# Performance work log

Hardware: AMD Instinct MI355X
Metric: run time of the kernel (lower is better)

## Reference

```python
import jax, jax.numpy as jnp
import numpy as np

B, T, C, H = 128, 256, 512, 512

def setup_inputs() -> dict:
    key = jax.random.key(0)
    k1, k2, k3, k4 = jax.random.split(key, 4)
    x = jax.random.normal(k1, (B, T, C), dtype=jnp.float32)
    # nn.Linear(n_embed, H_size, bias=False).weight has shape [H, C]; scaled init
    s = 1.0 / np.sqrt(C)
    Wq = jax.random.normal(k2, (H, C), dtype=jnp.float32) * s
    Wk = jax.random.normal(k3, (H, C), dtype=jnp.float32) * s
    Wv = jax.random.normal(k4, (H, C), dtype=jnp.float32) * s
    return {"x": x, "Wq": Wq, "Wk": Wk, "Wv": Wv}

def reference(x, Wq, Wk, Wv):
    # q,k,v: [B,T,H] = x @ W.T (torch Linear convention)
    q = jnp.einsum('btc,hc->bth', x, Wq)
    k = jnp.einsum('btc,hc->bth', x, Wk)
    v = jnp.einsum('btc,hc->bth', x, Wv)
    scale = k.shape[-1] ** -0.5
    score = jnp.einsum('bqh,bkh->bqk', q, k) * scale  # [B,T,T]
    # causal mask: position j attends to i only if i <= j
    i = jnp.arange(T)
    causal = i[None, :] <= i[:, None]  # [T,T] lower-triangular
    score = jnp.where(causal[None, :, :], score, -jnp.inf)
    attn = jax.nn.softmax(score, axis=-1)
    # dropout is identity in eval mode
    out = jnp.einsum('bqk,bkh->bqh', attn, v)  # [B,T,H]
    return out
```

## Files before the change

kernel.cpp:

```cpp
#include <hip/hip_runtime.h>

#define B_ 128
#define T_ 256
#define C_ 512
#define H_ 512
#define CSCALE 0.063763824f

typedef _Float16 f16x8 __attribute__((ext_vector_type(8)));
typedef _Float16 f16x4 __attribute__((ext_vector_type(4)));
typedef _Float16 f16x2 __attribute__((ext_vector_type(2)));
typedef float    f32x4 __attribute__((ext_vector_type(4)));
typedef float    f32x16 __attribute__((ext_vector_type(16)));
typedef unsigned int u32;
typedef u32 u32x4 __attribute__((ext_vector_type(4)));

__device__ __forceinline__ void gld16(const void* gsrc, void* ldst) {
  __builtin_amdgcn_global_load_lds(
      (__attribute__((address_space(1))) void*)gsrc,
      (__attribute__((address_space(3))) void*)ldst, 16, 0, 0);
}

__global__ __launch_bounds__(256) void cvtx_kernel(
    const float4* __restrict__ x, f16x4* __restrict__ dst) {
  const int NX = (B_ * T_ * C_) / 4;
  int gid = blockIdx.x * 256 + threadIdx.x;
  int gsz = gridDim.x * 256;
  for (int i = gid; i < NX; i += gsz) {
    float4 f = x[i];
    f16x4 u = {(_Float16)f.x, (_Float16)f.y, (_Float16)f.z, (_Float16)f.w};
    dst[i] = u;
  }
}

__global__ __launch_bounds__(256) void cvtw_kernel(
    const float4* __restrict__ wq, const float4* __restrict__ wk,
    const float4* __restrict__ wv, f16x4* __restrict__ dst) {
  const int NW = (H_ * C_) / 4;
  int i = blockIdx.x * 256 + threadIdx.x;
  if (i >= 3 * NW) return;
  float4 f = (i < NW) ? wq[i] : (i < 2 * NW ? wk[i - NW] : wv[i - 2 * NW]);
  f16x4 u = {(_Float16)f.x, (_Float16)f.y, (_Float16)f.z, (_Float16)f.w};
  dst[i] = u;
}

__global__ __launch_bounds__(256) void proj_kernel(
    const _Float16* __restrict__ xh, const _Float16* __restrict__ wh,
    _Float16* __restrict__ qh, _Float16* __restrict__ kh,
    _Float16* __restrict__ vth) {
  __shared__ _Float16 As[128 * 32];
  __shared__ _Float16 Bs[128 * 32];

  const int tid  = threadIdx.x;
  const int lane = tid & 63;
  const int wave = tid >> 6;
  const int lr = lane & 15, lk = lane >> 4;
  const int m0 = blockIdx.x * 128;
  const int n0 = blockIdx.y * 128;
  const int z  = blockIdx.z;
  const _Float16* wz = wh + z * (H_ * C_);

  const int wm = (wave >> 1) * 64;
  const int wn = (wave & 1) * 64;

  f32x4 acc[4][4];
#pragma unroll
  for (int i = 0; i < 4; ++i)
#pragma unroll
    for (int j = 0; j < 4; ++j) acc[i][j] = {0.f, 0.f, 0.f, 0.f};

  const int srow = tid >> 2, scol = (tid & 3) * 8;
  const _Float16* aSrc = xh + (size_t)(m0 + srow) * C_ + scol;
  const _Float16* bSrc = wz + (size_t)(n0 + srow) * C_ + scol;

  for (int k0 = 0; k0 < C_; k0 += 32) {
    __syncthreads();
#pragma unroll
    for (int i = 0; i < 2; ++i) {
      gld16((const void*)(aSrc + i * 64 * C_ + k0), (void*)&As[i * 2048 + wave * 512]);
      gld16((const void*)(bSrc + i * 64 * C_ + k0), (void*)&Bs[i * 2048 + wave * 512]);
    }
    __syncthreads();

    f16x8 a[4], b[4];
#pragma unroll
    for (int mi = 0; mi < 4; ++mi)
      a[mi] = *(const f16x8*)&As[(wm + mi * 16 + lr) * 32 + lk * 8];
#pragma unroll
    for (int ni = 0; ni < 4; ++ni)
      b[ni] = *(const f16x8*)&Bs[(wn + ni * 16 + lr) * 32 + lk * 8];
#pragma unroll
    for (int mi = 0; mi < 4; ++mi)
#pragma unroll
      for (int ni = 0; ni < 4; ++ni)
        acc[mi][ni] = __builtin_amdgcn_mfma_f32_16x16x32_f16(a[mi], b[ni], acc[mi][ni], 0, 0, 0);
  }

  if (z < 2) {
    _Float16* out = (z == 0) ? qh : kh;
#pragma unroll
    for (int mi = 0; mi < 4; ++mi) {
      int mbase = m0 + wm + mi * 16 + lk * 4;
#pragma unroll
      for (int ni = 0; ni < 4; ++ni) {
        int n = n0 + wn + ni * 16 + lr;
#pragma unroll
        for (int r = 0; r < 4; ++r)
          out[(size_t)(mbase + r) * H_ + n] = (_Float16)acc[mi][ni][r];
      }
    }
  } else {
#pragma unroll
    for (int mi = 0; mi < 4; ++mi) {
      int mbase = m0 + wm + mi * 16 + lk * 4;
      int bb = mbase >> 8, tt = mbase & 255;
#pragma unroll
      for (int ni = 0; ni < 4; ++ni) {
        int n = n0 + wn + ni * 16 + lr;
        f16x4 u = {(_Float16)acc[mi][ni][0], (_Float16)acc[mi][ni][1],
                   (_Float16)acc[mi][ni][2], (_Float16)acc[mi][ni][3]};
        *(f16x4*)&vth[(size_t)bb * (H_ * T_) + (size_t)n * T_ + tt] = u;
      }
    }
  }
}

__global__ __launch_bounds__(256, 3) void attn_kernel(
    const _Float16* __restrict__ qh, const _Float16* __restrict__ kh,
    const _Float16* __restrict__ vth, float* __restrict__ dout) {
  __shared__ f32x4 Ex[2][4][4][64];

  const int tid  = threadIdx.x;
  const int lane = tid & 63;
  const int wq   = tid >> 6;
  const int lq   = lane & 31;
  const int hi   = lane >> 5;
  const int flat = blockIdx.x;
  const int xcd  = flat & 7;
  const int rest = flat >> 3;
  const int qb   = 7 - (rest & 7);
  const int g    = rest >> 3;
  const int b    = xcd + (g << 3);
  const int q0   = qb * 32;
  const int nkv  = qb + 1;
  const int hbase = wq * 128;
  const int qg   = q0 + lq;

  f16x8 qf[8];
  const _Float16* qp = qh + ((size_t)b * T_ + qg) * H_ + hbase + hi * 8;
#pragma unroll
  for (int ks = 0; ks < 8; ++ks) qf[ks] = *(const f16x8*)&qp[ks * 16];

  f32x16 ot[4];
#pragma unroll
  for (int i = 0; i < 4; ++i) ot[i] = {};
  float m_ = -1e30f, l_ = 0.f;

  const _Float16* kp = kh  + ((size_t)b * T_ + lq) * H_ + hbase + hi * 8;
  const _Float16* vp = vth + ((size_t)b * H_ + hbase + lq) * T_ + hi * 8;

  {
    f32x16 s2 = {};
#pragma unroll
    for (int ks = 0; ks < 8; ++ks) {
      f16x8 kfv = *(const f16x8*)&kp[ks * 16];
      s2 = __builtin_amdgcn_mfma_f32_32x32x16_f16(kfv, qf[ks], s2, 0, 0, 0);
    }
#pragma unroll
    for (int c = 0; c < 4; ++c) {
      f32x4 w4 = {s2[c*4+0], s2[c*4+1], s2[c*4+2], s2[c*4+3]};
      Ex[0][wq][c][lane] = w4;
    }
  }

  for (int kvt = 0; kvt < nkv; ++kvt) {
    const int kv0 = kvt * 32;
    const int buf = kvt & 1;
    const bool more = (kvt + 1 < nkv);
    __syncthreads();

    f32x16 st;
#pragma unroll
    for (int c = 0; c < 4; ++c) {
      f32x4 r0 = Ex[buf][0][c][lane];
      f32x4 r1 = Ex[buf][1][c][lane];
      f32x4 r2 = Ex[buf][2][c][lane];
      f32x4 r3 = Ex[buf][3][c][lane];
      f32x4 r = (r0 + r1) + (r2 + r3);
      st[c*4+0] = r[0]; st[c*4+1] = r[1]; st[c*4+2] = r[2]; st[c*4+3] = r[3];
    }

    float rm = -1e30f;
    const int kvb = kv0 + 4 * hi;
#pragma unroll
    for (int r = 0; r < 16; ++r) {
      int kvg = kvb + (r & 3) + 8 * (r >> 2);
      float v = (kvg > qg) ? -1e30f : st[r];
      st[r] = v;
      rm = fmaxf(rm, v);
    }
    rm = fmaxf(rm, __shfl_xor(rm, 32, 64));

    if (__any((int)(rm > m_ + 64.f))) {
      float mn = fmaxf(m_, rm);
      float al = __builtin_amdgcn_exp2f((m_ - mn) * CSCALE);
      m_ = mn; l_ *= al;
#pragma unroll
      for (int i = 0; i < 4; ++i)
#pragma unroll
        for (int e = 0; e < 16; ++e) ot[i][e] *= al;
    }
    float rs = 0.f;
#pragma unroll
    for (int r = 0; r < 16; ++r) {
      st[r] = __builtin_amdgcn_exp2f((st[r] - m_) * CSCALE);
      rs += st[r];
    }
    rs += __shfl_xor(rs, 32, 64);
    l_ += rs;

    f16x8 pb0, pb1;
    {
      f16x2 h0 = {(_Float16)st[0], (_Float16)st[1]};
      f16x2 h1 = {(_Float16)st[2], (_Float16)st[3]};
      f16x2 h2 = {(_Float16)st[4], (_Float16)st[5]};
      f16x2 h3 = {(_Float16)st[6], (_Float16)st[7]};
      u32 w0 = __builtin_bit_cast(u32, h0), w1 = __builtin_bit_cast(u32, h1);
      u32 w2 = __builtin_bit_cast(u32, h2), w3 = __builtin_bit_cast(u32, h3);
      u32 s0 = (u32)__shfl_xor((int)w0, 32, 64);
      u32 s1 = (u32)__shfl_xor((int)w1, 32, 64);
      u32 s2 = (u32)__shfl_xor((int)w2, 32, 64);
      u32 s3 = (u32)__shfl_xor((int)w3, 32, 64);
      u32x4 t0 = { hi ? s2 : w0, hi ? s3 : w1, hi ? w2 : s0, hi ? w3 : s1 };
      pb0 = __builtin_bit_cast(f16x8, t0);
    }
    {
      f16x2 h0 = {(_Float16)st[8],  (_Float16)st[9]};
      f16x2 h1 = {(_Float16)st[10], (_Float16)st[11]};
      f16x2 h2 = {(_Float16)st[12], (_Float16)st[13]};
      f16x2 h3 = {(_Float16)st[14], (_Float16)st[15]};
      u32 w0 = __builtin_bit_cast(u32, h0), w1 = __builtin_bit_cast(u32, h1);
      u32 w2 = __builtin_bit_cast(u32, h2), w3 = __builtin_bit_cast(u32, h3);
      u32 s0 = (u32)__shfl_xor((int)w0, 32, 64);
      u32 s1 = (u32)__shfl_xor((int)w1, 32, 64);
      u32 s2 = (u32)__shfl_xor((int)w2, 32, 64);
      u32 s3 = (u32)__shfl_xor((int)w3, 32, 64);
      u32x4 t1 = { hi ? s2 : w0, hi ? s3 : w1, hi ? w2 : s0, hi ? w3 : s1 };
      pb1 = __builtin_bit_cast(f16x8, t1);
    }

    __builtin_amdgcn_s_setprio(1);
#pragma unroll
    for (int ht = 0; ht < 4; ++ht) {
      f16x8 va0 = *(const f16x8*)&vp[(size_t)(ht * 32) * T_ + kv0];
      f16x8 va1 = *(const f16x8*)&vp[(size_t)(ht * 32) * T_ + kv0 + 16];
      ot[ht] = __builtin_amdgcn_mfma_f32_32x32x16_f16(va0, pb0, ot[ht], 0, 0, 0);
      ot[ht] = __builtin_amdgcn_mfma_f32_32x32x16_f16(va1, pb1, ot[ht], 0, 0, 0);
    }
    __builtin_amdgcn_s_setprio(0);

    if (more) {
      f32x16 s2v = {};
      __builtin_amdgcn_s_setprio(1);
#pragma unroll
      for (int ks = 0; ks < 8; ++ks) {
        f16x8 kfv = *(const f16x8*)&kp[(size_t)(kv0 + 32) * H_ + ks * 16];
        s2v = __builtin_amdgcn_mfma_f32_32x32x16_f16(kfv, qf[ks], s2v, 0, 0, 0);
      }
      __builtin_amdgcn_s_setprio(0);
#pragma unroll
      for (int c = 0; c < 4; ++c) {
        f32x4 w4 = {s2v[c*4+0], s2v[c*4+1], s2v[c*4+2], s2v[c*4+3]};
        Ex[buf ^ 1][wq][c][lane] = w4;
      }
    }
  }

  float li = 1.0f / l_;
  float* op = dout + ((size_t)b * T_ + qg) * H_ + hbase + 4 * hi;
#pragma unroll
  for (int ht = 0; ht < 4; ++ht)
#pragma unroll
    for (int rq = 0; rq < 4; ++rq) {
      f32x4 v4 = {ot[ht][rq*4+0] * li, ot[ht][rq*4+1] * li,
                  ot[ht][rq*4+2] * li, ot[ht][rq*4+3] * li};
      *(f32x4*)&op[ht * 32 + rq * 8] = v4;
    }
}

extern "C" void kernel_launch(void* const* d_in, const int* in_sizes, int n_in,
                              void* d_out, int out_size, void* d_ws, size_t ws_size,
                              hipStream_t stream) {
  const size_t NXE = (size_t)B_ * T_ * C_;
  const size_t NWE = (size_t)3 * H_ * C_;
  const size_t NQE = (size_t)B_ * T_ * H_;
  const size_t need = (NXE + NWE + 3 * NQE) * sizeof(_Float16);
  if (ws_size < need) return;

  const float* x  = (const float*)d_in[0];
  const float* wq = (const float*)d_in[1];
  const float* wk = (const float*)d_in[2];
  const float* wv = (const float*)d_in[3];

  _Float16* xh  = (_Float16*)d_ws;
  _Float16* whh = xh + NXE;
  _Float16* qh  = whh + NWE;
  _Float16* kh  = qh + NQE;
  _Float16* vth = kh + NQE;

  cvtx_kernel<<<2048, 256, 0, stream>>>((const float4*)x, (f16x4*)xh);
  cvtw_kernel<<<768, 256, 0, stream>>>((const float4*)wq, (const float4*)wk,
                                       (const float4*)wv, (f16x4*)whh);
  proj_kernel<<<dim3(256, 4, 3), dim3(256), 0, stream>>>(xh, whh, qh, kh, vth);
  attn_kernel<<<1024, 256, 0, stream>>>(qh, kh, vth, (float*)d_out);
}
```

Baseline: 172.4 us.

## Restructure attention to stage K tiles in LDS and split waves by query and head

Replaces the per-wave head-split QK^T with a cross-wave LDS reduction by a layout where each wave owns 16 query rows and half of the head dimension for PV. K tiles are staged into swizzled, double-buffered LDS with async global-to-LDS loads. Each wave computes the full 512-wide QK^T with 16x16x32 MFMAs, which removes the fp32 partial-score exchange through shared memory. QK^T work is now duplicated across the two head-halves, occupancy drops to 2 blocks per SM, and register pressure from 16 Q fragments and 16 accumulators rises.

Measured after the change: 187.1 us. +8.5%, slower.

```diff
diff --git a/kernel.cpp b/kernel.cpp
--- a/kernel.cpp
+++ b/kernel.cpp
@@ -10,7 +10,6 @@
 typedef _Float16 f16x4 __attribute__((ext_vector_type(4)));
 typedef _Float16 f16x2 __attribute__((ext_vector_type(2)));
 typedef float    f32x4 __attribute__((ext_vector_type(4)));
-typedef float    f32x16 __attribute__((ext_vector_type(16)));
 typedef unsigned int u32;
 typedef u32 u32x4 __attribute__((ext_vector_type(4)));
 
@@ -124,16 +123,17 @@
   }
 }
 
-__global__ __launch_bounds__(256, 3) void attn_kernel(
+__global__ __launch_bounds__(256, 2) void attn_kernel(
     const _Float16* __restrict__ qh, const _Float16* __restrict__ kh,
     const _Float16* __restrict__ vth, float* __restrict__ dout) {
-  __shared__ f32x4 Ex[2][4][4][64];
+  __shared__ _Float16 Kl[2][32 * 512];
 
   const int tid  = threadIdx.x;
   const int lane = tid & 63;
-  const int wq   = tid >> 6;
-  const int lq   = lane & 31;
-  const int hi   = lane >> 5;
+  const int w    = tid >> 6;
+  const int lr = lane & 15, lk = lane >> 4;
+  const int qsub = w >> 1;
+  const int hh   = w & 1;
   const int flat = blockIdx.x;
   const int xcd  = flat & 7;
   const int rest = flat >> 3;
@@ -142,62 +142,65 @@
   const int b    = xcd + (g << 3);
   const int q0   = qb * 32;
   const int nkv  = qb + 1;
-  const int hbase = wq * 128;
-  const int qg   = q0 + lq;
-
-  f16x8 qf[8];
-  const _Float16* qp = qh + ((size_t)b * T_ + qg) * H_ + hbase + hi * 8;
-#pragma unroll
-  for (int ks = 0; ks < 8; ++ks) qf[ks] = *(const f16x8*)&qp[ks * 16];
-
-  f32x16 ot[4];
-#pragma unroll
-  for (int i = 0; i < 4; ++i) ot[i] = {};
+  const int qg   = q0 + qsub * 16 + lr;
+  const int h0   = hh * 256;
+
+  f16x8 qf[16];
+  const _Float16* qp = qh + ((size_t)b * T_ + qg) * H_ + lk * 8;
+#pragma unroll
+  for (int hs = 0; hs < 16; ++hs) qf[hs] = *(const f16x8*)&qp[hs * 32];
+
+  f32x4 ot[16];
+#pragma unroll
+  for (int i = 0; i < 16; ++i) ot[i] = {0.f, 0.f, 0.f, 0.f};
   float m_ = -1e30f, l_ = 0.f;
 
-  const _Float16* kp = kh  + ((size_t)b * T_ + lq) * H_ + hbase + hi * 8;
-  const _Float16* vp = vth + ((size_t)b * H_ + hbase + lq) * T_ + hi * 8;
-
-  {
-    f32x16 s2 = {};
-#pragma unroll
-    for (int ks = 0; ks < 8; ++ks) {
-      f16x8 kfv = *(const f16x8*)&kp[ks * 16];
-      s2 = __builtin_amdgcn_mfma_f32_32x32x16_f16(kfv, qf[ks], s2, 0, 0, 0);
-    }
-#pragma unroll
-    for (int c = 0; c < 4; ++c) {
-      f32x4 w4 = {s2[c*4+0], s2[c*4+1], s2[c*4+2], s2[c*4+3]};
-      Ex[0][wq][c][lane] = w4;
-    }
-  }
-
-  for (int kvt = 0; kvt < nkv; ++kvt) {
-    const int kv0 = kvt * 32;
-    const int buf = kvt & 1;
-    const bool more = (kvt + 1 < nkv);
-    __syncthreads();
-
-    f32x16 st;
-#pragma unroll
-    for (int c = 0; c < 4; ++c) {
-      f32x4 r0 = Ex[buf][0][c][lane];
-      f32x4 r1 = Ex[buf][1][c][lane];
-      f32x4 r2 = Ex[buf][2][c][lane];
-      f32x4 r3 = Ex[buf][3][c][lane];
-      f32x4 r = (r0 + r1) + (r2 + r3);
-      st[c*4+0] = r[0]; st[c*4+1] = r[1]; st[c*4+2] = r[2]; st[c*4+3] = r[3];
-    }
+  const _Float16* kbase = kh + (size_t)b * T_ * H_;
+  const _Float16* vp = vth + ((size_t)b * H_ + h0 + lr) * T_ + lk * 8;
+  const int swz = (lr & 7) << 3;
+
+#define KSTAGE(BUF, KV0) do {                                                 \
+    _Pragma("unroll") for (int i = 0; i < 8; ++i) {                            \
+      int kv = w * 8 + i;                                                      \
+      gld16((const void*)(kbase + ((size_t)((KV0) + kv)) * H_ +                \
+                          8 * (lane ^ (kv & 7))),                              \
+            (void*)&Kl[BUF][kv * 512]);                                        \
+    }                                                                          \
+  } while (0)
+
+  KSTAGE(0, 0);
+  __syncthreads();
+
+  for (int t = 0; t < nkv; ++t) {
+    const int kv0 = t * 32;
+    const int buf = t & 1;
+    if (t + 1 < nkv) KSTAGE(buf ^ 1, kv0 + 32);
+
+    f32x4 s0 = {0.f, 0.f, 0.f, 0.f}, s1 = {0.f, 0.f, 0.f, 0.f};
+#pragma unroll
+    for (int hs = 0; hs < 16; ++hs) {
+      int col = (hs * 32 + lk * 8) ^ swz;
+      f16x8 a0 = *(const f16x8*)&Kl[buf][lr * 512 + col];
+      f16x8 a1 = *(const f16x8*)&Kl[buf][(16 + lr) * 512 + col];
+      s0 = __builtin_amdgcn_mfma_f32_16x16x32_f16(a0, qf[hs], s0, 0, 0, 0);
+      s1 = __builtin_amdgcn_mfma_f32_16x16x32_f16(a1, qf[hs], s1, 0, 0, 0);
+    }
+
+    f16x8 vf[8];
+#pragma unroll
+    for (int hsub = 0; hsub < 8; ++hsub)
+      vf[hsub] = *(const f16x8*)&vp[(size_t)(hsub * 16) * T_ + kv0];
 
     float rm = -1e30f;
-    const int kvb = kv0 + 4 * hi;
-#pragma unroll
-    for (int r = 0; r < 16; ++r) {
-      int kvg = kvb + (r & 3) + 8 * (r >> 2);
-      float v = (kvg > qg) ? -1e30f : st[r];
-      st[r] = v;
-      rm = fmaxf(rm, v);
-    }
+#pragma unroll
+    for (int r = 0; r < 4; ++r) {
+      int kva = kv0 + lk * 4 + r;
+      float v0 = (kva > qg)      ? -1e30f : s0[r];
+      float v1 = (kva + 16 > qg) ? -1e30f : s1[r];
+      s0[r] = v0; s1[r] = v1;
+      rm = fmaxf(rm, fmaxf(v0, v1));
+    }
+    rm = fmaxf(rm, __shfl_xor(rm, 16, 64));
     rm = fmaxf(rm, __shfl_xor(rm, 32, 64));
 
     if (__any((int)(rm > m_ + 64.f))) {
@@ -205,86 +208,66 @@
       float al = __builtin_amdgcn_exp2f((m_ - mn) * CSCALE);
       m_ = mn; l_ *= al;
 #pragma unroll
-      for (int i = 0; i < 4; ++i)
-#pragma unroll
-        for (int e = 0; e < 16; ++e) ot[i][e] *= al;
+      for (int i = 0; i < 16; ++i)
+#pragma unroll
+        for (int e = 0; e < 4; ++e) ot[i][e] *= al;
     }
     float rs = 0.f;
 #pragma unroll
-    for (int r = 0; r < 16; ++r) {
-      st[r] = __builtin_amdgcn_exp2f((st[r] - m_) * CSCALE);
-      rs += st[r];
-    }
+    for (int r = 0; r < 4; ++r) {
+      s0[r] = __builtin_amdgcn_exp2f((s0[r] - m_) * CSCALE);
+      s1[r] = __builtin_amdgcn_exp2f((s1[r] - m_) * CSCALE);
+      rs += s0[r] + s1[r];
+    }
+    rs += __shfl_xor(rs, 16, 64);
     rs += __shfl_xor(rs, 32, 64);
     l_ += rs;
 
-    f16x8 pb0, pb1;
+    f16x8 pb;
     {
-      f16x2 h0 = {(_Float16)st[0], (_Float16)st[1]};
-      f16x2 h1 = {(_Float16)st[2], (_Float16)st[3]};
-      f16x2 h2 = {(_Float16)st[4], (_Float16)st[5]};
-      f16x2 h3 = {(_Float16)st[6], (_Float16)st[7]};
-      u32 w0 = __builtin_bit_cast(u32, h0), w1 = __builtin_bit_cast(u32, h1);
-      u32 w2 = __builtin_bit_cast(u32, h2), w3 = __builtin_bit_cast(u32, h3);
-      u32 s0 = (u32)__shfl_xor((int)w0, 32, 64);
-      u32 s1 = (u32)__shfl_xor((int)w1, 32, 64);
-      u32 s2 = (u32)__shfl_xor((int)w2, 32, 64);
-      u32 s3 = (u32)__shfl_xor((int)w3, 32, 64);
-      u32x4 t0 = { hi ? s2 : w0, hi ? s3 : w1, hi ? w2 : s0, hi ? w3 : s1 };
-      pb0 = __builtin_bit_cast(f16x8, t0);
-    }
-    {
-      f16x2 h0 = {(_Float16)st[8],  (_Float16)st[9]};
-      f16x2 h1 = {(_Float16)st[10], (_Float16)st[11]};
-      f16x2 h2 = {(_Float16)st[12], (_Float16)st[13]};
-      f16x2 h3 = {(_Float16)st[14], (_Float16)st[15]};
-      u32 w0 = __builtin_bit_cast(u32, h0), w1 = __builtin_bit_cast(u32, h1);
-      u32 w2 = __builtin_bit_cast(u32, h2), w3 = __builtin_bit_cast(u32, h3);
-      u32 s0 = (u32)__shfl_xor((int)w0, 32, 64);
-      u32 s1 = (u32)__shfl_xor((int)w1, 32, 64);
-      u32 s2 = (u32)__shfl_xor((int)w2, 32, 64);
-      u32 s3 = (u32)__shfl_xor((int)w3, 32, 64);
-      u32x4 t1 = { hi ? s2 : w0, hi ? s3 : w1, hi ? w2 : s0, hi ? w3 : s1 };
-      pb1 = __builtin_bit_cast(f16x8, t1);
+      f16x2 p0 = {(_Float16)s0[0], (_Float16)s0[1]};
+      f16x2 p1 = {(_Float16)s0[2], (_Float16)s0[3]};
+      f16x2 p2 = {(_Float16)s1[0], (_Float16)s1[1]};
+      f16x2 p3 = {(_Float16)s1[2], (_Float16)s1[3]};
+      u32 u0 = __builtin_bit_cast(u32, p0), u1 = __builtin_bit_cast(u32, p1);
+      u32 u2 = __builtin_bit_cast(u32, p2), u3 = __builtin_bit_cast(u32, p3);
+      int srcA = ((lk & 1) << 5) | lr;
+      int srcB = srcA + 16;
+      u32 a0 = (u32)__shfl((int)u0, srcA, 64);
+      u32 a1 = (u32)__shfl((int)u1, srcA, 64);
+      u32 a2 = (u32)__shfl((int)u2, srcA, 64);
+      u32 a3 = (u32)__shfl((int)u3, srcA, 64);
+      u32 b0 = (u32)__shfl((int)u0, srcB, 64);
+      u32 b1 = (u32)__shfl((int)u1, srcB, 64);
+      u32 b2 = (u32)__shfl((int)u2, srcB, 64);
+      u32 b3 = (u32)__shfl((int)u3, srcB, 64);
+      bool X = (lk >> 1) & 1;
+      u32x4 tt = { X ? a2 : a0, X ? a3 : a1, X ? b2 : b0, X ? b3 : b1 };
+      pb = __builtin_bit_cast(f16x8, tt);
     }
 
     __builtin_amdgcn_s_setprio(1);
 #pragma unroll
-    for (int ht = 0; ht < 4; ++ht) {
-      f16x8 va0 = *(const f16x8*)&vp[(size_t)(ht * 32) * T_ + kv0];
-      f16x8 va1 = *(const f16x8*)&vp[(size_t)(ht * 32) * T_ + kv0 + 16];
-      ot[ht] = __builtin_amdgcn_mfma_f32_32x32x16_f16(va0, pb0, ot[ht], 0, 0, 0);
-      ot[ht] = __builtin_amdgcn_mfma_f32_32x32x16_f16(va1, pb1, ot[ht], 0, 0, 0);
+    for (int hsub = 0; hsub < 8; ++hsub)
+      ot[hsub] = __builtin_amdgcn_mfma_f32_16x16x32_f16(vf[hsub], pb, ot[hsub], 0, 0, 0);
+#pragma unroll
+    for (int hsub = 8; hsub < 16; ++hsub) {
+      f16x8 va = *(const f16x8*)&vp[(size_t)(hsub * 16) * T_ + kv0];
+      ot[hsub] = __builtin_amdgcn_mfma_f32_16x16x32_f16(va, pb, ot[hsub], 0, 0, 0);
     }
     __builtin_amdgcn_s_setprio(0);
 
-    if (more) {
-      f32x16 s2v = {};
-      __builtin_amdgcn_s_setprio(1);
-#pragma unroll
-      for (int ks = 0; ks < 8; ++ks) {
-        f16x8 kfv = *(const f16x8*)&kp[(size_t)(kv0 + 32) * H_ + ks * 16];
-        s2v = __builtin_amdgcn_mfma_f32_32x32x16_f16(kfv, qf[ks], s2v, 0, 0, 0);
-      }
-      __builtin_amdgcn_s_setprio(0);
-#pragma unroll
-      for (int c = 0; c < 4; ++c) {
-        f32x4 w4 = {s2v[c*4+0], s2v[c*4+1], s2v[c*4+2], s2v[c*4+3]};
-        Ex[buf ^ 1][wq][c][lane] = w4;
-      }
-    }
+    __syncthreads();
   }
 
   float li = 1.0f / l_;
-  float* op = dout + ((size_t)b * T_ + qg) * H_ + hbase + 4 * hi;
-#pragma unroll
-  for (int ht = 0; ht < 4; ++ht)
-#pragma unroll
-    for (int rq = 0; rq < 4; ++rq) {
-      f32x4 v4 = {ot[ht][rq*4+0] * li, ot[ht][rq*4+1] * li,
-                  ot[ht][rq*4+2] * li, ot[ht][rq*4+3] * li};
-      *(f32x4*)&op[ht * 32 + rq * 8] = v4;
-    }
+  float* op = dout + ((size_t)b * T_ + qg) * H_ + h0 + lk * 4;
+#pragma unroll
+  for (int hsub = 0; hsub < 16; ++hsub) {
+    f32x4 v4 = {ot[hsub][0] * li, ot[hsub][1] * li,
+                ot[hsub][2] * li, ot[hsub][3] * li};
+    *(f32x4*)&op[hsub * 16] = v4;
+  }
 }
 
 extern "C" void kernel_launch(void* const* d_in, const int* in_sizes, int n_in,
```
